# Kernel tuning notes

Measured on AMD Instinct MI355X. Metric: run time of the kernel, lower is better.

Reference implementation:

```python
import jax, jax.numpy as jnp
import numpy as np
import math

COV_WEIGHT = 1.0
BANDWIDTH_FACTOR = 1.06
SQRT_2PI = math.sqrt(2.0 * math.pi)
EPS_LOG = 1e-8
H_MIN = 1e-4


def setup_inputs() -> dict:
    key = jax.random.key(0)
    activity = jax.random.normal(key, (2048, 64), dtype=jnp.float32)
    return {"activity": activity}


def reference(activity):
    B, R = activity.shape
    # Silverman bandwidth per receptor (torch .std uses ddof=1)
    std = jnp.std(activity, axis=0, ddof=1)                     # (R,)
    h = jnp.maximum(BANDWIDTH_FACTOR * std * (B ** (-0.2)), H_MIN)  # (R,)

    # Pairwise Gaussian KDE: query == samples == activity
    u = (activity[:, None, :] - activity[None, :, :]) / h       # (B_q, B_s, R)
    kernel_values = jnp.exp(-0.5 * u * u) / SQRT_2PI             # (B_q, B_s, R)
    density = kernel_values.sum(axis=1) / (B * h)                # (B_q, R)

    entropies = -jnp.mean(jnp.log(density + EPS_LOG), axis=0)    # (R,)
    loss_entropy = -entropies.mean()

    # Covariance penalty: sum of squared off-diagonals
    centered = activity - activity.mean(axis=0, keepdims=True)
    cov = (centered.T @ centered) / (B - 1)                      # (R, R)
    off = cov - jnp.diag(jnp.diag(cov))
    loss_cov = jnp.sum(off * off)

    total_loss = loss_entropy + COV_WEIGHT * loss_cov
    return total_loss
```

## Files before the change

### kernel.cpp

```cpp
#include <hip/hip_runtime.h>
#include <math.h>

#define B_SZ 2048
#define R_SZ 64
#define QT 8
#define KDE_BLOCKS (B_SZ / QT)

#define B_POW_NEG02 0.217637640824031f
#define SQRT_2PI 2.5066282746310002f
#define LOG2E 1.44269504088896340736f

extern "C" __device__ float __ocml_native_exp2_f32(float);

typedef __attribute__((ext_vector_type(2))) float f32x2;


__global__ __launch_bounds__(1024) void cov_stats_kernel(const float* __restrict__ A,
                                                         float* __restrict__ U,
                                                         float* __restrict__ lscale,
                                                         float* __restrict__ cov_partial,
                                                         float* __restrict__ ent_acc,
                                                         int* __restrict__ done_cnt) {
    int i = blockIdx.x;
    int tid = threadIdx.x;
    int j = tid & 63, bg = tid >> 6;

    float g = 0.f, sj = 0.f, s2j = 0.f;
#pragma unroll 4
    for (int b = bg; b < B_SZ; b += 16) {
        float ai = A[b * R_SZ + i];
        float aj = A[b * R_SZ + j];
        g = fmaf(ai, aj, g);
        sj += aj;
        s2j = fmaf(aj, aj, s2j);
    }

    __shared__ float gred[16][64], sred[16][64], s2red[16][64];
    __shared__ float gfin[64], sfin[64], hs[64];
    gred[bg][j] = g; sred[bg][j] = sj; s2red[bg][j] = s2j;
    __syncthreads();
    if (tid < 64) {
        float G = 0.f, S = 0.f, S2 = 0.f;
#pragma unroll
        for (int t = 0; t < 16; ++t) { G += gred[t][j]; S += sred[t][j]; S2 += s2red[t][j]; }
        gfin[j] = G;
        sfin[j] = S;
        float m = S * (1.f / (float)B_SZ);
        float var = (S2 - S * m) * (1.f / (float)(B_SZ - 1));
        var = fmaxf(var, 0.f);
        float h = fmaxf(1.06f * sqrtf(var) * B_POW_NEG02, 1e-4f);
        hs[j] = sqrtf(0.5f * LOG2E) / h;
        if (i == 0) lscale[j] = 1.0f / ((float)B_SZ * h * SQRT_2PI);
    }
    __syncthreads();
    if (tid < 64) {
        float m_j = sfin[j] * (1.f / (float)B_SZ);
        float m_i = sfin[i] * (1.f / (float)B_SZ);
        float cov = (gfin[j] - (float)B_SZ * m_i * m_j) * (1.f / (float)(B_SZ - 1));
        float v = (j == i) ? 0.f : cov * cov;
        for (int off = 32; off > 0; off >>= 1) v += __shfl_down(v, off, 64);
        if (j == 0) cov_partial[i] = v;
    }
    if (i == 0 && tid == 64) { *ent_acc = 0.f; *done_cnt = 0; }

    int base = i * (32 * R_SZ);
    float k0 = hs[tid & 63];
    U[base + tid]        = A[base + tid]        * k0;
    U[base + 1024 + tid] = A[base + 1024 + tid] * k0;
}

__global__ __launch_bounds__(1024) void kde_kernel(const float* __restrict__ U,
                                                   const float* __restrict__ lscale,
                                                   const float* __restrict__ cov_partial,
                                                   float* __restrict__ ent_acc,
                                                   int* __restrict__ done_cnt,
                                                   float* __restrict__ out) {
    int tid = threadIdx.x;
    int r = tid & 63, sg = tid >> 6;
    int q0 = blockIdx.x * QT;

    f32x2 uq01 = { U[(q0 + 0) * R_SZ + r], U[(q0 + 1) * R_SZ + r] };
    f32x2 uq23 = { U[(q0 + 2) * R_SZ + r], U[(q0 + 3) * R_SZ + r] };
    f32x2 uq45 = { U[(q0 + 4) * R_SZ + r], U[(q0 + 5) * R_SZ + r] };
    f32x2 uq67 = { U[(q0 + 6) * R_SZ + r], U[(q0 + 7) * R_SZ + r] };
    f32x2 c01 = { 0.f, 0.f }, c23 = { 0.f, 0.f };
    f32x2 c45 = { 0.f, 0.f }, c67 = { 0.f, 0.f };

#define KDE_BODY(usv)                                                          \
    {                                                                          \
        f32x2 uss = { (usv), (usv) };                                          \
        f32x2 d01 = uq01 - uss, d23 = uq23 - uss;                              \
        f32x2 d45 = uq45 - uss, d67 = uq67 - uss;                              \
        f32x2 n01 = -d01 * d01, n23 = -d23 * d23;                              \
        f32x2 n45 = -d45 * d45, n67 = -d67 * d67;                              \
        f32x2 e01 = { __ocml_native_exp2_f32(n01.x), __ocml_native_exp2_f32(n01.y) }; \
        f32x2 e23 = { __ocml_native_exp2_f32(n23.x), __ocml_native_exp2_f32(n23.y) }; \
        f32x2 e45 = { __ocml_native_exp2_f32(n45.x), __ocml_native_exp2_f32(n45.y) }; \
        f32x2 e67 = { __ocml_native_exp2_f32(n67.x), __ocml_native_exp2_f32(n67.y) }; \
        c01 += e01; c23 += e23; c45 += e45; c67 += e67;                        \
    }

    const float* Up = U + sg * R_SZ + r;
    float p[8];
#pragma unroll
    for (int j = 0; j < 8; ++j) p[j] = Up[j * 1024];

    int li = 8 * 1024;
#pragma unroll 1
    for (int k = 0; k < 15; ++k) {
#pragma unroll
        for (int j = 0; j < 8; ++j) {
            float us = p[j];
            p[j] = Up[li + j * 1024];
            KDE_BODY(us);
        }
        li += 8 * 1024;
    }
#pragma unroll
    for (int j = 0; j < 8; ++j) KDE_BODY(p[j]);

#undef KDE_BODY

    __shared__ float red[16][QT][64];
    red[sg][0][r] = c01.x; red[sg][1][r] = c01.y;
    red[sg][2][r] = c23.x; red[sg][3][r] = c23.y;
    red[sg][4][r] = c45.x; red[sg][5][r] = c45.y;
    red[sg][6][r] = c67.x; red[sg][7][r] = c67.y;
    __syncthreads();
    __shared__ float wred[QT];
    if (sg < QT) {
        float S = 0.f;
#pragma unroll
        for (int t = 0; t < 16; ++t) S += red[t][sg][r];
        float v = __logf(fmaf(S, lscale[r], 1e-8f));
        for (int off = 32; off > 0; off >>= 1) v += __shfl_down(v, off, 64);
        if (r == 0) wred[sg] = v;
    }
    __syncthreads();
    __shared__ int lastflag;
    if (tid == 0) {
        float p2 = 0.f;
#pragma unroll
        for (int t = 0; t < QT; ++t) p2 += wred[t];
        p2 *= (1.0f / ((float)B_SZ * (float)R_SZ));
        atomicAdd(ent_acc, p2);
        __threadfence();
        int prev = atomicAdd(done_cnt, 1);
        lastflag = (prev == KDE_BLOCKS - 1);
    }
    __syncthreads();
    if (lastflag && tid < 64) {
        __threadfence();
        float v = cov_partial[tid];
        for (int off = 32; off > 0; off >>= 1) v += __shfl_down(v, off, 64);
        if (tid == 0) {
            float ent = __hip_atomic_load(ent_acc, __ATOMIC_ACQUIRE,
                                          __HIP_MEMORY_SCOPE_AGENT);
            out[0] = ent + v;
        }
    }
}

extern "C" void kernel_launch(void* const* d_in, const int* in_sizes, int n_in,
                              void* d_out, int out_size, void* d_ws, size_t ws_size,
                              hipStream_t stream) {
    const float* A = (const float*)d_in[0];
    float* out = (float*)d_out;

    float* wsf = (float*)d_ws;
    float* lscale      = wsf;
    float* cov_partial = wsf + 64;
    float* ent_acc     = wsf + 160;
    int*   done_cnt    = (int*)(wsf + 192);
    float* U           = wsf + 256;

    cov_stats_kernel<<<R_SZ, 1024, 0, stream>>>(A, U, lscale, cov_partial,
                                                ent_acc, done_cnt);
    kde_kernel<<<KDE_BLOCKS, 1024, 0, stream>>>(U, lscale, cov_partial,
                                                ent_acc, done_cnt, out);
}
```

Measured before the change: 99.02 us.

## Split KDE sample range across two blocks and add separate entropy kernel

Each query tile's sample loop is split across two blocks, doubling the grid to raise occupancy and latency hiding. Partial densities are accumulated with float atomics into a zeroed density buffer. Log/entropy reduction moves to a new third kernel that does the final cross-block combine. This adds a kernel launch, extra global traffic and atomic contention in exchange for more parallelism.

Measured after the change: 100.3 us. Within noise of the previous version (+1.3%).

```diff
diff --git a/kernel.cpp b/kernel.cpp
--- a/kernel.cpp
+++ b/kernel.cpp
@@ -4,7 +4,8 @@
 #define B_SZ 2048
 #define R_SZ 64
 #define QT 8
-#define KDE_BLOCKS (B_SZ / QT)
+#define NSPLIT 2
+#define KDE_BLOCKS (B_SZ / QT * NSPLIT)
 
 #define B_POW_NEG02 0.217637640824031f
 #define SQRT_2PI 2.5066282746310002f
@@ -17,10 +18,11 @@
 
 __global__ __launch_bounds__(1024) void cov_stats_kernel(const float* __restrict__ A,
                                                          float* __restrict__ U,
+                                                         float* __restrict__ density,
                                                          float* __restrict__ lscale,
                                                          float* __restrict__ cov_partial,
                                                          float* __restrict__ ent_acc,
-                                                         int* __restrict__ done_cnt) {
+                                                         int* __restrict__ done2) {
     int i = blockIdx.x;
     int tid = threadIdx.x;
     int j = tid & 63, bg = tid >> 6;
@@ -61,23 +63,23 @@
         for (int off = 32; off > 0; off >>= 1) v += __shfl_down(v, off, 64);
         if (j == 0) cov_partial[i] = v;
     }
-    if (i == 0 && tid == 64) { *ent_acc = 0.f; *done_cnt = 0; }
+    if (i == 0 && tid == 64) { *ent_acc = 0.f; *done2 = 0; }
 
     int base = i * (32 * R_SZ);
     float k0 = hs[tid & 63];
     U[base + tid]        = A[base + tid]        * k0;
     U[base + 1024 + tid] = A[base + 1024 + tid] * k0;
+    density[base + tid] = 0.f;
+    density[base + 1024 + tid] = 0.f;
 }
 
 __global__ __launch_bounds__(1024) void kde_kernel(const float* __restrict__ U,
-                                                   const float* __restrict__ lscale,
-                                                   const float* __restrict__ cov_partial,
-                                                   float* __restrict__ ent_acc,
-                                                   int* __restrict__ done_cnt,
-                                                   float* __restrict__ out) {
+                                                   float* __restrict__ density) {
     int tid = threadIdx.x;
     int r = tid & 63, sg = tid >> 6;
-    int q0 = blockIdx.x * QT;
+    int g = blockIdx.x >> 1;
+    int half = blockIdx.x & 1;
+    int q0 = g * QT;
 
     f32x2 uq01 = { U[(q0 + 0) * R_SZ + r], U[(q0 + 1) * R_SZ + r] };
     f32x2 uq23 = { U[(q0 + 2) * R_SZ + r], U[(q0 + 3) * R_SZ + r] };
@@ -100,14 +102,14 @@
         c01 += e01; c23 += e23; c45 += e45; c67 += e67;                        \
     }
 
-    const float* Up = U + sg * R_SZ + r;
+    const float* Up = U + (half * 1024 + sg) * R_SZ + r;
     float p[8];
 #pragma unroll
     for (int j = 0; j < 8; ++j) p[j] = Up[j * 1024];
 
     int li = 8 * 1024;
 #pragma unroll 1
-    for (int k = 0; k < 15; ++k) {
+    for (int k = 0; k < 7; ++k) {
 #pragma unroll
         for (int j = 0; j < 8; ++j) {
             float us = p[j];
@@ -127,36 +129,49 @@
     red[sg][4][r] = c45.x; red[sg][5][r] = c45.y;
     red[sg][6][r] = c67.x; red[sg][7][r] = c67.y;
     __syncthreads();
-    __shared__ float wred[QT];
     if (sg < QT) {
         float S = 0.f;
 #pragma unroll
         for (int t = 0; t < 16; ++t) S += red[t][sg][r];
-        float v = __logf(fmaf(S, lscale[r], 1e-8f));
-        for (int off = 32; off > 0; off >>= 1) v += __shfl_down(v, off, 64);
-        if (r == 0) wred[sg] = v;
+        unsafeAtomicAdd(&density[(q0 + sg) * R_SZ + r], S);
     }
+}
+
+__global__ __launch_bounds__(1024) void entropy_kernel(const float* __restrict__ density,
+                                                       const float* __restrict__ lscale,
+                                                       const float* __restrict__ cov_partial,
+                                                       float* __restrict__ ent_acc,
+                                                       int* __restrict__ done2,
+                                                       float* __restrict__ out) {
+    int tid = threadIdx.x;
+    int r = tid & 63, sg = tid >> 6;
+    float ls = lscale[r];
+    int f = blockIdx.x * 2048 + tid;
+    float v = __logf(fmaf(density[f], ls, 1e-8f))
+            + __logf(fmaf(density[f + 1024], ls, 1e-8f));
+    for (int off = 32; off > 0; off >>= 1) v += __shfl_down(v, off, 64);
+    __shared__ float wr[16];
+    if (r == 0) wr[sg] = v;
     __syncthreads();
     __shared__ int lastflag;
     if (tid == 0) {
-        float p2 = 0.f;
+        float s = 0.f;
 #pragma unroll
-        for (int t = 0; t < QT; ++t) p2 += wred[t];
-        p2 *= (1.0f / ((float)B_SZ * (float)R_SZ));
-        atomicAdd(ent_acc, p2);
+        for (int w = 0; w < 16; ++w) s += wr[w];
+        atomicAdd(ent_acc, s);
         __threadfence();
-        int prev = atomicAdd(done_cnt, 1);
-        lastflag = (prev == KDE_BLOCKS - 1);
+        int prev = atomicAdd(done2, 1);
+        lastflag = (prev == 63);
     }
     __syncthreads();
     if (lastflag && tid < 64) {
         __threadfence();
-        float v = cov_partial[tid];
-        for (int off = 32; off > 0; off >>= 1) v += __shfl_down(v, off, 64);
+        float v2 = cov_partial[tid];
+        for (int off = 32; off > 0; off >>= 1) v2 += __shfl_down(v2, off, 64);
         if (tid == 0) {
             float ent = __hip_atomic_load(ent_acc, __ATOMIC_ACQUIRE,
                                           __HIP_MEMORY_SCOPE_AGENT);
-            out[0] = ent + v;
+            out[0] = ent * (1.0f / ((float)B_SZ * (float)R_SZ)) + v2;
         }
     }
 }
@@ -171,11 +186,13 @@
     float* lscale      = wsf;
     float* cov_partial = wsf + 64;
     float* ent_acc     = wsf + 160;
-    int*   done_cnt    = (int*)(wsf + 192);
+    int*   done2       = (int*)(wsf + 192);
     float* U           = wsf + 256;
+    float* density     = wsf + 256 + B_SZ * R_SZ;
 
-    cov_stats_kernel<<<R_SZ, 1024, 0, stream>>>(A, U, lscale, cov_partial,
-                                                ent_acc, done_cnt);
-    kde_kernel<<<KDE_BLOCKS, 1024, 0, stream>>>(U, lscale, cov_partial,
-                                                ent_acc, done_cnt, out);
+    cov_stats_kernel<<<R_SZ, 1024, 0, stream>>>(A, U, density, lscale, cov_partial,
+                                                ent_acc, done2);
+    kde_kernel<<<KDE_BLOCKS, 1024, 0, stream>>>(U, density);
+    entropy_kernel<<<64, 1024, 0, stream>>>(density, lscale, cov_partial,
+                                            ent_acc, done2, out);
 }
```
